# Optimization experiments

Measured on AMD Instinct MI355X. Metric: run time of the kernel, lower is better.

Reference implementation:

```python
import jax, jax.numpy as jnp
import numpy as np
import math

N_HEAD = 16

def _c(a):
    # stack real/imag -> complex64
    return jax.lax.complex(a[..., 0], a[..., 1])

def _rope_phasor(T, D, dtype=jnp.float32):
    inv_freq = 1.0 / (10000.0 ** (jnp.arange(D, dtype=dtype) / D))
    t = jnp.arange(T, dtype=dtype)
    freqs = jnp.outer(t, inv_freq)  # [T, D]
    return jax.lax.complex(jnp.cos(freqs), jnp.sin(freqs))

def setup_inputs() -> dict:
    key = jax.random.key(0)
    ks = jax.random.split(key, 9)
    B, T, C = 2, 1024, 1024
    s = 0.02
    return {
        "x":  jax.random.normal(ks[0], (B, T, C, 2), jnp.float32),
        "wq": jax.random.normal(ks[1], (C, C, 2), jnp.float32) * s,
        "bq": jax.random.normal(ks[2], (C, 2), jnp.float32) * s,
        "wk": jax.random.normal(ks[3], (C, C, 2), jnp.float32) * s,
        "bk": jax.random.normal(ks[4], (C, 2), jnp.float32) * s,
        "wv": jax.random.normal(ks[5], (C, C, 2), jnp.float32) * s,
        "bv": jax.random.normal(ks[6], (C, 2), jnp.float32) * s,
        "wo": jax.random.normal(ks[7], (C, C, 2), jnp.float32) * s,
        "bo": jax.random.normal(ks[8], (C, 2), jnp.float32) * s,
    }

def reference(x, wq, bq, wk, bk, wv, bv, wo, bo):
    B, T, C, _ = x.shape
    H = N_HEAD
    D = C // H
    xc = _c(x)
    # complex linear projections: y = x @ W^T + b
    q = xc @ _c(wq).T + _c(bq)
    k = xc @ _c(wk).T + _c(bk)
    v = xc @ _c(wv).T + _c(bv)
    # [B, T, C] -> [B, H, T, D]
    q = q.reshape(B, T, H, D).transpose(0, 2, 1, 3)
    k = k.reshape(B, T, H, D).transpose(0, 2, 1, 3)
    v = v.reshape(B, T, H, D).transpose(0, 2, 1, 3)
    # complex RoPE phasor multiply
    ph = _rope_phasor(T, D)[None, None]  # [1,1,T,D]
    q = q * ph
    k = k * ph
    # complex QK^H, scaled
    score = jnp.einsum('bhtd,bhsd->bhts', q, jnp.conj(k)) / math.sqrt(D)
    # softmax over magnitude, then real-valued complex weights
    attn = jax.nn.softmax(jnp.abs(score), axis=-1)
    attn_c = jax.lax.complex(attn, jnp.zeros_like(attn))
    out = jnp.einsum('bhts,bhsd->bhtd', attn_c, v)
    out = out.transpose(0, 2, 1, 3).reshape(B, T, C)
    out = out @ _c(wo).T + _c(bo)
    # return real/imag stacked for a real-valued harness
    return jnp.stack([out.real, out.imag], axis=-1)
```

## Files before the change

### kernel.cpp

```cpp
#include <hip/hip_runtime.h>
#include <math.h>

#define T_SEQ  1024
#define C_DIM  1024
#define NH_    16
#define H_DIM  64
#define SCL    (0.125f * 1.4426950408889634f)

typedef __bf16 bf16;
typedef __bf16 bf16x4 __attribute__((ext_vector_type(4)));
typedef __bf16 bf16x8 __attribute__((ext_vector_type(8)));
typedef float  f32x4  __attribute__((ext_vector_type(4)));

template<bool B> struct BC { static constexpr bool value = B; };

#define MFMA16(a, b, c) __builtin_amdgcn_mfma_f32_16x16x32_bf16(a, b, c, 0, 0, 0)

#define GLOAD_LDS16(g, l) __builtin_amdgcn_global_load_lds( \
    (const __attribute__((address_space(1))) void*)(g),     \
    (__attribute__((address_space(3))) void*)(l), 16, 0, 0)

__device__ __forceinline__ bf16x8 neg8(bf16x8 x) {
    union { bf16x8 v; unsigned int u[4]; } t;
    t.v = x;
    t.u[0] ^= 0x80008000u; t.u[1] ^= 0x80008000u;
    t.u[2] ^= 0x80008000u; t.u[3] ^= 0x80008000u;
    return t.v;
}

__device__ __forceinline__ bf16x8 frag_sw(const bf16* plane, int row, int chunk) {
    int c = chunk ^ (row & 7);
    return *(const bf16x8*)&plane[row * 64 + c * 8];
}
__device__ __forceinline__ bf16x8 frag_sw4(const bf16* plane, int row, int chunk) {
    int c = chunk ^ (row & 3);
    return *(const bf16x8*)&plane[row * 32 + c * 8];
}
__device__ __forceinline__ bf16x8 frag_sw4b(const bf16* plane, int row, int chunk) {
    int c = chunk ^ ((row >> 1) & 3);
    return *(const bf16x8*)&plane[row * 32 + c * 8];
}

__global__ __launch_bounds__(256)
void split_all(const float* __restrict__ x,  const float* __restrict__ wq,
               const float* __restrict__ wk, const float* __restrict__ wv,
               const float* __restrict__ wo,
               bf16* Xr, bf16* Xi, bf16* Wqr, bf16* Wqi, bf16* Wkr, bf16* Wki,
               bf16* Wvr, bf16* Wvi, bf16* Wor, bf16* Woi,
               float* __restrict__ rope)
{
    int z = blockIdx.y;
    if (z == 5) {
        if (blockIdx.x >= 256) return;
        int idx = blockIdx.x * 256 + threadIdx.x;
        int tp = idx >> 6, d = idx & 63;
        float invf = exp2f((float)d * -0.2076205059304601f);
        float fr = (float)tp * invf;
        float sn, cs; sincosf(fr, &sn, &cs);
        *(float2*)&rope[(size_t)idx * 2] = make_float2(cs, sn);
        return;
    }
    if (z > 0 && blockIdx.x >= 512) return;
    const float* in; bf16 *pr, *pi;
    if      (z == 0) { in = x;  pr = Xr;  pi = Xi;  }
    else if (z == 1) { in = wq; pr = Wqr; pi = Wqi; }
    else if (z == 2) { in = wk; pr = Wkr; pi = Wki; }
    else if (z == 3) { in = wv; pr = Wvr; pi = Wvi; }
    else             { in = wo; pr = Wor; pi = Woi; }
    int idx = (blockIdx.x * 256 + threadIdx.x) * 8;
    bf16x8 r, im;
#pragma unroll
    for (int j = 0; j < 4; j++) {
        float4 v = *(const float4*)(in + (size_t)idx * 2 + j * 4);
        r[2*j]   = (bf16)v.x; im[2*j]   = (bf16)v.y;
        r[2*j+1] = (bf16)v.z; im[2*j+1] = (bf16)v.w;
    }
    *(bf16x8*)(pr + idx) = r;
    *(bf16x8*)(pi + idx) = im;
}

__global__ __launch_bounds__(512, 2)
void qkv_gemm(const bf16* __restrict__ Xr, const bf16* __restrict__ Xi,
              const bf16* __restrict__ Wqr, const bf16* __restrict__ Wqi,
              const bf16* __restrict__ Wkr, const bf16* __restrict__ Wki,
              const bf16* __restrict__ Wvr, const bf16* __restrict__ Wvi,
              const float* __restrict__ bq, const float* __restrict__ bk,
              const float* __restrict__ bv, const float* __restrict__ rope,
              bf16* Qr, bf16* Qi, bf16* Kr, bf16* Ki, bf16* Vr, bf16* Vi)
{
    __shared__ __attribute__((aligned(16))) bf16 smem[61440];
    const int t = threadIdx.x, lane = t & 63, wave = t >> 6;
    const int wm = (wave >> 1) * 32, wn = (wave & 1) * 32;
    const int lm = lane & 15, quad = lane >> 4;
    const int lr4 = lane >> 2, sc4q = ((lane & 3) ^ ((lane >> 3) & 3)) * 8;
    const int h = blockIdx.x, m0 = blockIdx.y * 128, n0 = h * 64;

    auto stage1 = [&](bf16* bb_, int j, int k0) {
        int c = wave + 8 * j;
        const bf16* src; bf16* dst;
        if (c < 8)       {                 src = Xr  + (size_t)(m0 + c * 16 + lr4) * C_DIM + k0 + sc4q; dst = bb_ + c * 512; }
        else if (c < 16) { int u = c - 8;  src = Xi  + (size_t)(m0 + u * 16 + lr4) * C_DIM + k0 + sc4q; dst = bb_ + 4096  + u * 512; }
        else if (c < 20) { int u = c - 16; src = Wqr + (size_t)(n0 + u * 16 + lr4) * C_DIM + k0 + sc4q; dst = bb_ + 8192  + u * 512; }
        else if (c < 24) { int u = c - 20; src = Wqi + (size_t)(n0 + u * 16 + lr4) * C_DIM + k0 + sc4q; dst = bb_ + 10240 + u * 512; }
        else if (c < 28) { int u = c - 24; src = Wkr + (size_t)(n0 + u * 16 + lr4) * C_DIM + k0 + sc4q; dst = bb_ + 12288 + u * 512; }
        else if (c < 32) { int u = c - 28; src = Wki + (size_t)(n0 + u * 16 + lr4) * C_DIM + k0 + sc4q; dst = bb_ + 14336 + u * 512; }
        else if (c < 36) { int u = c - 32; src = Wvr + (size_t)(n0 + u * 16 + lr4) * C_DIM + k0 + sc4q; dst = bb_ + 16384 + u * 512; }
        else             { int u = c - 36; src = Wvi + (size_t)(n0 + u * 16 + lr4) * C_DIM + k0 + sc4q; dst = bb_ + 18432 + u * 512; }
        GLOAD_LDS16(src, dst);
    };

    f32x4 accr[3][2][2], acci[3][2][2];
#pragma unroll
    for (int p = 0; p < 3; p++)
#pragma unroll
        for (int i = 0; i < 2; i++)
#pragma unroll
            for (int j = 0; j < 2; j++) { accr[p][i][j] = (f32x4)0.f; acci[p][i][j] = (f32x4)0.f; }

    auto step = [&](auto DOSTAGE, auto DRAIN, int bufsel, int sbsel, int k2) {
        const bf16* buf = smem + bufsel * 20480;
        bf16* sb = smem + sbsel * 20480;
        if constexpr (DRAIN.value)
            asm volatile("s_waitcnt vmcnt(0)\n\ts_barrier" ::: "memory");
        else
            asm volatile("s_waitcnt vmcnt(5)\n\ts_barrier" ::: "memory");

        bf16x8 ar[2], ai_[2], br_[2], bi_[2], bn_[2];
#pragma unroll
        for (int i = 0; i < 2; i++) {
            ar[i]  = frag_sw4b(buf,        wm + i * 16 + lm, quad);
            ai_[i] = frag_sw4b(buf + 4096, wm + i * 16 + lm, quad);
        }
#pragma unroll
        for (int j = 0; j < 2; j++) {
            br_[j] = frag_sw4b(buf + 8192,  wn + j * 16 + lm, quad);
            bi_[j] = frag_sw4b(buf + 10240, wn + j * 16 + lm, quad);
        }
        if constexpr (DOSTAGE.value) { stage1(sb, 0, k2); stage1(sb, 1, k2); }
        asm volatile("s_waitcnt lgkmcnt(0)" ::: "memory");
        __builtin_amdgcn_sched_barrier(0);
        __builtin_amdgcn_s_setprio(1);
#pragma unroll
        for (int j = 0; j < 2; j++) bn_[j] = neg8(bi_[j]);
#pragma unroll
        for (int i = 0; i < 2; i++)
#pragma unroll
            for (int j = 0; j < 2; j++) {
                accr[0][i][j] = MFMA16(ar[i],  br_[j], accr[0][i][j]);
                accr[0][i][j] = MFMA16(ai_[i], bn_[j], accr[0][i][j]);
                acci[0][i][j] = MFMA16(ar[i],  bi_[j], acci[0][i][j]);
                acci[0][i][j] = MFMA16(ai_[i], br_[j], acci[0][i][j]);
            }
        __builtin_amdgcn_s_setprio(0);
        __builtin_amdgcn_s_barrier();
#pragma unroll
        for (int j = 0; j < 2; j++) {
            br_[j] = frag_sw4b(buf + 12288, wn + j * 16 + lm, quad);
            bi_[j] = frag_sw4b(buf + 14336, wn + j * 16 + lm, quad);
        }
        if constexpr (DOSTAGE.value) { stage1(sb, 2, k2); stage1(sb, 3, k2); }
        asm volatile("s_waitcnt lgkmcnt(0)" ::: "memory");
        __builtin_amdgcn_sched_barrier(0);
        __builtin_amdgcn_s_setprio(1);
#pragma unroll
        for (int j = 0; j < 2; j++) bn_[j] = neg8(bi_[j]);
#pragma unroll
        for (int i = 0; i < 2; i++)
#pragma unroll
            for (int j = 0; j < 2; j++) {
                accr[1][i][j] = MFMA16(ar[i],  br_[j], accr[1][i][j]);
                accr[1][i][j] = MFMA16(ai_[i], bn_[j], accr[1][i][j]);
                acci[1][i][j] = MFMA16(ar[i],  bi_[j], acci[1][i][j]);
                acci[1][i][j] = MFMA16(ai_[i], br_[j], acci[1][i][j]);
            }
        __builtin_amdgcn_s_setprio(0);
        __builtin_amdgcn_s_barrier();
#pragma unroll
        for (int j = 0; j < 2; j++) {
            br_[j] = frag_sw4b(buf + 16384, wn + j * 16 + lm, quad);
            bi_[j] = frag_sw4b(buf + 18432, wn + j * 16 + lm, quad);
        }
        if constexpr (DOSTAGE.value) { stage1(sb, 4, k2); }
        asm volatile("s_waitcnt lgkmcnt(0)" ::: "memory");
        __builtin_amdgcn_sched_barrier(0);
        __builtin_amdgcn_s_setprio(1);
#pragma unroll
        for (int j = 0; j < 2; j++) bn_[j] = neg8(bi_[j]);
#pragma unroll
        for (int i = 0; i < 2; i++)
#pragma unroll
            for (int j = 0; j < 2; j++) {
                accr[2][i][j] = MFMA16(ar[i],  br_[j], accr[2][i][j]);
                accr[2][i][j] = MFMA16(ai_[i], bn_[j], accr[2][i][j]);
                acci[2][i][j] = MFMA16(ar[i],  bi_[j], acci[2][i][j]);
                acci[2][i][j] = MFMA16(ai_[i], br_[j], acci[2][i][j]);
            }
        __builtin_amdgcn_s_setprio(0);
    };

#pragma unroll
    for (int j = 0; j < 5; j++) stage1(smem,         j, 0);
#pragma unroll
    for (int j = 0; j < 5; j++) stage1(smem + 20480, j, 32);

    for (int base = 0; base < 30; base += 3) {
        step(BC<true>{}, BC<false>{}, 0, 2, (base + 2) * 32);
        step(BC<true>{}, BC<false>{}, 1, 0, (base + 3) * 32);
        step(BC<true>{}, BC<false>{}, 2, 1, (base + 4) * 32);
    }
    step(BC<false>{}, BC<false>{}, 0, 0, 0);
    step(BC<false>{}, BC<true >{}, 1, 0, 0);

    const int bb = m0 >> 10, tbase = m0 & (T_SEQ - 1);

#pragma unroll
    for (int p = 0; p < 2; p++) {
        const float* bias = p ? bk : bq;
#pragma unroll
        for (int i = 0; i < 2; i++)
#pragma unroll
            for (int j = 0; j < 2; j++) {
                int d = wn + j * 16 + lm;
                float2 bvv = *(const float2*)&bias[2 * (n0 + d)];
#pragma unroll
                for (int r = 0; r < 4; r++) {
                    int tpos = tbase + wm + i * 16 + quad * 4 + r;
                    float2 ph = *(const float2*)&rope[((size_t)tpos * H_DIM + d) * 2];
                    float yr = accr[p][i][j][r] + bvv.x;
                    float yi = acci[p][i][j][r] + bvv.y;
                    accr[p][i][j][r] = yr * ph.x - yi * ph.y;
                    acci[p][i][j][r] = yr * ph.y + yi * ph.x;
                }
            }
        bf16* dr = (p ? Kr : Qr) + ((size_t)(bb * NH_ + h) * T_SEQ + tbase) * H_DIM;
        bf16* di = (p ? Ki : Qi) + ((size_t)(bb * NH_ + h) * T_SEQ + tbase) * H_DIM;
#pragma unroll
        for (int pass = 0; pass < 2; pass++) {
            __syncthreads();
#pragma unroll
            for (int i = 0; i < 2; i++)
#pragma unroll
                for (int j = 0; j < 2; j++)
#pragma unroll
                    for (int r = 0; r < 4; r++)
                        smem[(wm + i * 16 + quad * 4 + r) * 72 + wn + j * 16 + lm] =
                            (bf16)(pass ? acci[p][i][j][r] : accr[p][i][j][r]);
            __syncthreads();
            bf16* dst = pass ? di : dr;
#pragma unroll
            for (int pp = 0; pp < 2; pp++) {
                int ch = t + 512 * pp;
                int row = ch >> 3, o = (ch & 7) * 8;
                *(bf16x8*)&dst[row * H_DIM + o] = *(const bf16x8*)&smem[row * 72 + o];
            }
        }
    }

    {
#pragma unroll
        for (int pass = 0; pass < 2; pass++) {
            __syncthreads();
#pragma unroll
            for (int i = 0; i < 2; i++)
#pragma unroll
                for (int j = 0; j < 2; j++) {
                    int d = wn + j * 16 + lm;
                    float2 bvv = *(const float2*)&bv[2 * (n0 + d)];
                    float bb2 = pass ? bvv.y : bvv.x;
                    bf16x4 pk;
#pragma unroll
                    for (int r = 0; r < 4; r++)
                        pk[r] = (bf16)((pass ? acci[2][i][j][r] : accr[2][i][j][r]) + bb2);
                    *(bf16x4*)&smem[d * 136 + wm + i * 16 + quad * 4] = pk;
                }
            __syncthreads();
            bf16* dst = (pass ? Vi : Vr) + ((size_t)(bb * NH_ + h) * H_DIM) * T_SEQ + tbase;
#pragma unroll
            for (int pp = 0; pp < 2; pp++) {
                int ch = t + 512 * pp;
                int row = ch >> 4, o = (ch & 15) * 8;
                *(bf16x8*)&dst[(size_t)row * T_SEQ + o] = *(const bf16x8*)&smem[row * 136 + o];
            }
        }
    }
}

__global__ __launch_bounds__(256, 4)
void out_gemm(const bf16* __restrict__ Ar, const bf16* __restrict__ Ai,
              const bf16* __restrict__ Br, const bf16* __restrict__ Bi,
              const float* __restrict__ bias, float* __restrict__ Y)
{
    __shared__ __attribute__((aligned(16))) bf16 sm[16384];
    const int t = threadIdx.x, lane = t & 63, wave = t >> 6;
    const int lm = lane & 15, quad = lane >> 4;
    const int s_lr = lane >> 3, s_c = (lane & 7) ^ s_lr;
    const int wm = (wave >> 1) * 32, wn = (wave & 1) * 32;
    const int m0 = blockIdx.y * 64, n0 = blockIdx.x * 64;

    f32x4 accr[2][2], acci[2][2];
#pragma unroll
    for (int i = 0; i < 2; i++)
#pragma unroll
        for (int j = 0; j < 2; j++) { accr[i][j] = (f32x4)0.f; acci[i][j] = (f32x4)0.f; }

    for (int k0 = 0; k0 < C_DIM; k0 += 64) {
#pragma unroll
        for (int j = 0; j < 8; j++) {
            int c = wave + 4 * j;
            const bf16* src; bf16* dst;
            if (c < 8)       {             src = Ar + (size_t)(m0 + c * 8 + s_lr) * C_DIM + k0 + s_c * 8; dst = sm + c * 512; }
            else if (c < 16) { int u = c - 8;  src = Ai + (size_t)(m0 + u * 8 + s_lr) * C_DIM + k0 + s_c * 8; dst = sm + 4096 + u * 512; }
            else if (c < 24) { int u = c - 16; src = Br + (size_t)(n0 + u * 8 + s_lr) * C_DIM + k0 + s_c * 8; dst = sm + 8192 + u * 512; }
            else             { int u = c - 24; src = Bi + (size_t)(n0 + u * 8 + s_lr) * C_DIM + k0 + s_c * 8; dst = sm + 12288 + u * 512; }
            GLOAD_LDS16(src, dst);
        }
        __syncthreads();
#pragma unroll
        for (int kh = 0; kh < 2; kh++) {
            bf16x8 ar[2], ai_[2], br_[2], bi_[2], bn_[2];
#pragma unroll
            for (int i = 0; i < 2; i++) {
                ar[i]  = frag_sw(sm,        wm + i * 16 + lm, kh * 4 + quad);
                ai_[i] = frag_sw(sm + 4096, wm + i * 16 + lm, kh * 4 + quad);
            }
#pragma unroll
            for (int j = 0; j < 2; j++) {
                br_[j] = frag_sw(sm + 8192,  wn + j * 16 + lm, kh * 4 + quad);
                bi_[j] = frag_sw(sm + 12288, wn + j * 16 + lm, kh * 4 + quad);
                bn_[j] = neg8(bi_[j]);
            }
#pragma unroll
            for (int i = 0; i < 2; i++)
#pragma unroll
                for (int j = 0; j < 2; j++) {
                    accr[i][j] = MFMA16(ar[i],  br_[j], accr[i][j]);
                    accr[i][j] = MFMA16(ai_[i], bn_[j], accr[i][j]);
                    acci[i][j] = MFMA16(ar[i],  bi_[j], acci[i][j]);
                    acci[i][j] = MFMA16(ai_[i], br_[j], acci[i][j]);
                }
        }
        __syncthreads();
    }
#pragma unroll
    for (int i = 0; i < 2; i++)
#pragma unroll
        for (int j = 0; j < 2; j++) {
            int n = n0 + wn + j * 16 + lm;
            float2 bvv = *(const float2*)&bias[2 * n];
#pragma unroll
            for (int r = 0; r < 4; r++) {
                int m = m0 + wm + i * 16 + quad * 4 + r;
                *(float2*)&Y[((size_t)m * C_DIM + n) * 2] =
                    make_float2(accr[i][j][r] + bvv.x, acci[i][j][r] + bvv.y);
            }
        }
}

__global__ __launch_bounds__(512, 4)
void attn_mfma(const bf16* __restrict__ Qpr, const bf16* __restrict__ Qpi,
               const bf16* __restrict__ Kpr, const bf16* __restrict__ Kpi,
               const bf16* __restrict__ Vtr, const bf16* __restrict__ Vti,
               bf16* __restrict__ ABr, bf16* __restrict__ ABi)
{
    __shared__ __attribute__((aligned(16))) bf16 smem[32768];
    const int t = threadIdx.x, lane = t & 63, w = t >> 6;
    const int qg = w & 3, sh = w >> 2;
    const int lm = lane & 15, quad = lane >> 4;
    const int q0 = blockIdx.x * 64;
    const int h = blockIdx.y, b = blockIdx.z;
    const size_t hb = (size_t)(b * NH_ + h) * T_SEQ * H_DIM;
    const int s_lr = lane >> 3, s_c = (lane & 7) ^ s_lr;
    const int lr4 = lane >> 2, sc4a = ((lane & 3) ^ (lr4 & 3)) * 8;

    {
        const bf16* gq = (sh ? Qpi : Qpr) + hb + (size_t)q0 * H_DIM;
        bf16* lq = smem + 16384 + sh * 4096;
#pragma unroll
        for (int j = 0; j < 2; j++) {
            int cc = qg * 2 + j;
            GLOAD_LDS16(gq + (cc * 8 + s_lr) * H_DIM + s_c * 8, lq + cc * 512);
        }
    }
    __syncthreads();

    bf16x8 qfr[2], qfi[2], nqfr[2];
#pragma unroll
    for (int kh = 0; kh < 2; kh++) {
        qfr[kh]  = frag_sw(smem + 16384, qg * 16 + lm, kh * 4 + quad);
        qfi[kh]  = frag_sw(smem + 20480, qg * 16 + lm, kh * 4 + quad);
        nqfr[kh] = neg8(qfr[kh]);
    }

#pragma unroll
    for (int pre = 0; pre < 1; pre++) {
        const int S = sh * 512;
        bf16* bd = smem + sh * 8192;
        if (qg < 2) {
            const bf16* g = (qg ? Kpi : Kpr) + hb + (size_t)S * H_DIM;
            bf16* d = bd + (qg ? 2048 : 0);
#pragma unroll
            for (int cc = 0; cc < 4; cc++)
                GLOAD_LDS16(g + (cc * 8 + s_lr) * H_DIM + s_c * 8, d + cc * 512);
        } else {
            const bf16* g = (qg == 2 ? Vtr : Vti) + hb + S;
            bf16* d = bd + (qg == 2 ? 4096 : 6144);
#pragma unroll
            for (int cc = 0; cc < 4; cc++)
                GLOAD_LDS16(g + (size_t)(cc * 16 + lr4) * T_SEQ + sc4a, d + cc * 512);
        }
    }

    f32x4 Or[4], Oi[4];
#pragma unroll
    for (int nt = 0; nt < 4; nt++) { Or[nt] = (f32x4)0.f; Oi[nt] = (f32x4)0.f; }
    float lsum = 0.f;
    const int idxA = (((2 * quad) & 3) * 16 + lm) * 4;
    const int idxB = idxA + 64;
    const bool hisel = quad >= 2;

    for (int it = 0; it < 16; it++) {
        __syncthreads();
        if (it < 15) {
            const int S = (it + 1) * 32 + sh * 512;
            bf16* bd = smem + ((it + 1) & 1) * 16384 + sh * 8192;
            if (qg < 2) {
                const bf16* g = (qg ? Kpi : Kpr) + hb + (size_t)S * H_DIM;
                bf16* d = bd + (qg ? 2048 : 0);
#pragma unroll
                for (int cc = 0; cc < 4; cc++)
                    GLOAD_LDS16(g + (cc * 8 + s_lr) * H_DIM + s_c * 8, d + cc * 512);
            } else {
                const bf16* g = (qg == 2 ? Vtr : Vti) + hb + S;
                bf16* d = bd + (qg == 2 ? 4096 : 6144);
#pragma unroll
                for (int cc = 0; cc < 4; cc++)
                    GLOAD_LDS16(g + (size_t)(cc * 16 + lr4) * T_SEQ + sc4a, d + cc * 512);
            }
        }
        const bf16* buf = smem + (it & 1) * 16384 + sh * 8192;

        union { unsigned int u[2]; bf16 b[4]; } pk[2];
        float lsA = 0.f, lsB = 0.f;
#pragma unroll
        for (int ct = 0; ct < 2; ct++) {
            f32x4 sre = (f32x4)0.f, sim = (f32x4)0.f;
            __builtin_amdgcn_s_setprio(1);
#pragma unroll
            for (int kh = 0; kh < 2; kh++) {
                bf16x8 kr = frag_sw(buf,        ct * 16 + lm, kh * 4 + quad);
                bf16x8 ki = frag_sw(buf + 2048, ct * 16 + lm, kh * 4 + quad);
                sre = MFMA16(kr, qfr[kh],  sre);
                sre = MFMA16(ki, qfi[kh],  sre);
                sim = MFMA16(kr, qfi[kh],  sim);
                sim = MFMA16(ki, nqfr[kh], sim);
            }
            __builtin_amdgcn_s_setprio(0);
#pragma unroll
            for (int r = 0; r < 4; r++) {
                float mag2 = fmaf(sre[r], sre[r], sim[r] * sim[r]);
                float p = __builtin_amdgcn_exp2f(__builtin_amdgcn_sqrtf(mag2) * SCL);
                if (ct) lsB += p; else lsA += p;
                pk[ct].b[r] = (bf16)p;
            }
        }
        lsum += lsA + lsB;

        union { unsigned int u[4]; bf16x8 v; } pf;
        {
            int a0 = __builtin_amdgcn_ds_bpermute(idxA, (int)pk[0].u[0]);
            int a1 = __builtin_amdgcn_ds_bpermute(idxA, (int)pk[1].u[0]);
            int b0 = __builtin_amdgcn_ds_bpermute(idxA, (int)pk[0].u[1]);
            int b1 = __builtin_amdgcn_ds_bpermute(idxA, (int)pk[1].u[1]);
            int c0 = __builtin_amdgcn_ds_bpermute(idxB, (int)pk[0].u[0]);
            int c1 = __builtin_amdgcn_ds_bpermute(idxB, (int)pk[1].u[0]);
            int d0 = __builtin_amdgcn_ds_bpermute(idxB, (int)pk[0].u[1]);
            int d1 = __builtin_amdgcn_ds_bpermute(idxB, (int)pk[1].u[1]);
            pf.u[0] = (unsigned int)(hisel ? a1 : a0);
            pf.u[1] = (unsigned int)(hisel ? b1 : b0);
            pf.u[2] = (unsigned int)(hisel ? c1 : c0);
            pf.u[3] = (unsigned int)(hisel ? d1 : d0);
        }

        __builtin_amdgcn_s_setprio(1);
#pragma unroll
        for (int nt = 0; nt < 4; nt++) {
            Or[nt] = MFMA16(pf.v, frag_sw4(buf + 4096, nt * 16 + lm, quad), Or[nt]);
            Oi[nt] = MFMA16(pf.v, frag_sw4(buf + 6144, nt * 16 + lm, quad), Oi[nt]);
        }
        __builtin_amdgcn_s_setprio(0);
    }

    lsum += __shfl_xor(lsum, 16);
    lsum += __shfl_xor(lsum, 32);

    __syncthreads();
    float* Of  = (float*)smem;
    float* lsc = Of + 128 * 66;
    if (sh == 1) {
#pragma unroll
        for (int nt = 0; nt < 4; nt++)
#pragma unroll
            for (int r = 0; r < 4; r++) {
                Of[((qg * 2 + 0) * 16 + quad * 4 + r) * 66 + nt * 16 + lm] = Or[nt][r];
                Of[((qg * 2 + 1) * 16 + quad * 4 + r) * 66 + nt * 16 + lm] = Oi[nt][r];
            }
        if (quad == 0) lsc[qg * 16 + lm] = lsum;
    }
    __syncthreads();
    if (sh == 0) {
        float ltot = lsum + lsc[qg * 16 + lm];
        float lv = 1.f / ltot;
        float linv[4];
#pragma unroll
        for (int r = 0; r < 4; r++)
            linv[r] = __shfl(lv, (quad << 4) + quad * 4 + r, 64);
        size_t mbase = (size_t)(b * T_SEQ + q0 + qg * 16 + quad * 4) * C_DIM;
        int colb = h * H_DIM + lm;
#pragma unroll
        for (int nt = 0; nt < 4; nt++)
#pragma unroll
            for (int r = 0; r < 4; r++) {
                float orv = Or[nt][r] + Of[((qg * 2 + 0) * 16 + quad * 4 + r) * 66 + nt * 16 + lm];
                float oiv = Oi[nt][r] + Of[((qg * 2 + 1) * 16 + quad * 4 + r) * 66 + nt * 16 + lm];
                size_t o = mbase + (size_t)r * C_DIM + colb + nt * 16;
                ABr[o] = (bf16)(orv * linv[r]);
                ABi[o] = (bf16)(oiv * linv[r]);
            }
    }
}

extern "C" void kernel_launch(void* const* d_in, const int* in_sizes, int n_in,
                              void* d_out, int out_size, void* d_ws, size_t ws_size,
                              hipStream_t stream) {
    const float* x  = (const float*)d_in[0];
    const float* wq = (const float*)d_in[1];
    const float* bq = (const float*)d_in[2];
    const float* wk = (const float*)d_in[3];
    const float* bk = (const float*)d_in[4];
    const float* wv = (const float*)d_in[5];
    const float* bv = (const float*)d_in[6];
    const float* wo = (const float*)d_in[7];
    const float* bo = (const float*)d_in[8];

    float* rope = (float*)d_ws;
    bf16* w = (bf16*)(rope + 131072);
    const size_t MSZ = (size_t)2048 * 1024;
    const size_t WSZ = (size_t)1024 * 1024;
    const size_t PSZ = (size_t)2 * NH_ * T_SEQ * H_DIM;

    bf16 *Xr = w, *Xi = Xr + MSZ;
    bf16 *Wqr = Xi + MSZ,  *Wqi = Wqr + WSZ;
    bf16 *Wkr = Wqi + WSZ, *Wki = Wkr + WSZ;
    bf16 *Wvr = Wki + WSZ, *Wvi = Wvr + WSZ;
    bf16 *Wor = Wvi + WSZ, *Woi = Wor + WSZ;
    bf16 *Qr = Woi + WSZ, *Qi = Qr + PSZ;
    bf16 *Kr = Qi + PSZ,  *Ki = Kr + PSZ;
    bf16 *Vr = Ki + PSZ,  *Vi = Vr + PSZ;
    bf16 *ABr = Vi + PSZ, *ABi = ABr + MSZ;

    split_all<<<dim3(1024, 6), 256, 0, stream>>>(x, wq, wk, wv, wo,
        Xr, Xi, Wqr, Wqi, Wkr, Wki, Wvr, Wvi, Wor, Woi, rope);

    qkv_gemm<<<dim3(16, 16), 512, 0, stream>>>(
        Xr, Xi, Wqr, Wqi, Wkr, Wki, Wvr, Wvi, bq, bk, bv, rope,
        Qr, Qi, Kr, Ki, Vr, Vi);

    attn_mfma<<<dim3(16, 16, 2), 512, 0, stream>>>(
        Qr, Qi, Kr, Ki, Vr, Vi, ABr, ABi);

    out_gemm<<<dim3(16, 32), 256, 0, stream>>>(ABr, ABi, Wor, Woi, bo, (float*)d_out);
}
```

Before: 210.4 us.

## Double-buffer QKV GEMM LDS for two blocks per CU; remap attention grid

The QKV projection GEMM drops its three-stage LDS ring (120 KB) for a simple two-buffer loop (80 KB). Each iteration now waits for all outstanding loads before computing. The smaller LDS footprint should let two 512-thread blocks share a CU, as the launch bounds request, so one block's compute can hide the other's memory latency. The cost is that the per-block prefetch distance shrinks. Separately, the attention kernel now takes the head from blockIdx.x and the query tile from blockIdx.y, which changes block dispatch order and the cache locality of K/V reads across concurrently running blocks.

```diff
diff --git a/kernel.cpp b/kernel.cpp
--- a/kernel.cpp
+++ b/kernel.cpp
@@ -11,8 +11,6 @@
 typedef __bf16 bf16x4 __attribute__((ext_vector_type(4)));
 typedef __bf16 bf16x8 __attribute__((ext_vector_type(8)));
 typedef float  f32x4  __attribute__((ext_vector_type(4)));
-
-template<bool B> struct BC { static constexpr bool value = B; };
 
 #define MFMA16(a, b, c) __builtin_amdgcn_mfma_f32_16x16x32_bf16(a, b, c, 0, 0, 0)
 
@@ -88,7 +86,7 @@
               const float* __restrict__ bv, const float* __restrict__ rope,
               bf16* Qr, bf16* Qi, bf16* Kr, bf16* Ki, bf16* Vr, bf16* Vi)
 {
-    __shared__ __attribute__((aligned(16))) bf16 smem[61440];
+    __shared__ __attribute__((aligned(16))) bf16 smem[40960];
     const int t = threadIdx.x, lane = t & 63, wave = t >> 6;
     const int wm = (wave >> 1) * 32, wn = (wave & 1) * 32;
     const int lm = lane & 15, quad = lane >> 4;
@@ -117,13 +115,15 @@
 #pragma unroll
             for (int j = 0; j < 2; j++) { accr[p][i][j] = (f32x4)0.f; acci[p][i][j] = (f32x4)0.f; }
 
-    auto step = [&](auto DOSTAGE, auto DRAIN, int bufsel, int sbsel, int k2) {
-        const bf16* buf = smem + bufsel * 20480;
-        bf16* sb = smem + sbsel * 20480;
-        if constexpr (DRAIN.value)
-            asm volatile("s_waitcnt vmcnt(0)\n\ts_barrier" ::: "memory");
-        else
-            asm volatile("s_waitcnt vmcnt(5)\n\ts_barrier" ::: "memory");
+#pragma unroll
+    for (int j = 0; j < 5; j++) stage1(smem, j, 0);
+
+    for (int it = 0; it < 32; it++) {
+        asm volatile("s_waitcnt vmcnt(0)\n\ts_barrier" ::: "memory");
+        const bf16* buf = smem + (it & 1) * 20480;
+        bf16* sb = smem + ((it + 1) & 1) * 20480;
+        const bool dostage = it < 31;
+        const int k2 = (it + 1) * 32;
 
         bf16x8 ar[2], ai_[2], br_[2], bi_[2], bn_[2];
 #pragma unroll
@@ -136,7 +136,7 @@
             br_[j] = frag_sw4b(buf + 8192,  wn + j * 16 + lm, quad);
             bi_[j] = frag_sw4b(buf + 10240, wn + j * 16 + lm, quad);
         }
-        if constexpr (DOSTAGE.value) { stage1(sb, 0, k2); stage1(sb, 1, k2); }
+        if (dostage) { stage1(sb, 0, k2); stage1(sb, 1, k2); }
         asm volatile("s_waitcnt lgkmcnt(0)" ::: "memory");
         __builtin_amdgcn_sched_barrier(0);
         __builtin_amdgcn_s_setprio(1);
@@ -158,7 +158,7 @@
             br_[j] = frag_sw4b(buf + 12288, wn + j * 16 + lm, quad);
             bi_[j] = frag_sw4b(buf + 14336, wn + j * 16 + lm, quad);
         }
-        if constexpr (DOSTAGE.value) { stage1(sb, 2, k2); stage1(sb, 3, k2); }
+        if (dostage) { stage1(sb, 2, k2); stage1(sb, 3, k2); }
         asm volatile("s_waitcnt lgkmcnt(0)" ::: "memory");
         __builtin_amdgcn_sched_barrier(0);
         __builtin_amdgcn_s_setprio(1);
@@ -180,7 +180,7 @@
             br_[j] = frag_sw4b(buf + 16384, wn + j * 16 + lm, quad);
             bi_[j] = frag_sw4b(buf + 18432, wn + j * 16 + lm, quad);
         }
-        if constexpr (DOSTAGE.value) { stage1(sb, 4, k2); }
+        if (dostage) { stage1(sb, 4, k2); }
         asm volatile("s_waitcnt lgkmcnt(0)" ::: "memory");
         __builtin_amdgcn_sched_barrier(0);
         __builtin_amdgcn_s_setprio(1);
@@ -196,20 +196,7 @@
                 acci[2][i][j] = MFMA16(ai_[i], br_[j], acci[2][i][j]);
             }
         __builtin_amdgcn_s_setprio(0);
-    };
-
-#pragma unroll
-    for (int j = 0; j < 5; j++) stage1(smem,         j, 0);
-#pragma unroll
-    for (int j = 0; j < 5; j++) stage1(smem + 20480, j, 32);
-
-    for (int base = 0; base < 30; base += 3) {
-        step(BC<true>{}, BC<false>{}, 0, 2, (base + 2) * 32);
-        step(BC<true>{}, BC<false>{}, 1, 0, (base + 3) * 32);
-        step(BC<true>{}, BC<false>{}, 2, 1, (base + 4) * 32);
-    }
-    step(BC<false>{}, BC<false>{}, 0, 0, 0);
-    step(BC<false>{}, BC<true >{}, 1, 0, 0);
+    }
 
     const int bb = m0 >> 10, tbase = m0 & (T_SEQ - 1);
 
@@ -366,8 +353,9 @@
     const int t = threadIdx.x, lane = t & 63, w = t >> 6;
     const int qg = w & 3, sh = w >> 2;
     const int lm = lane & 15, quad = lane >> 4;
-    const int q0 = blockIdx.x * 64;
-    const int h = blockIdx.y, b = blockIdx.z;
+    const int h = blockIdx.x;
+    const int q0 = blockIdx.y * 64;
+    const int b = blockIdx.z;
     const size_t hb = (size_t)(b * NH_ + h) * T_SEQ * H_DIM;
     const int s_lr = lane >> 3, s_c = (lane & 7) ^ s_lr;
     const int lr4 = lane >> 2, sc4a = ((lane & 3) ^ (lr4 & 3)) * 8;
```

Result: faster. 205.0 us (-2.5%).
